# Kernel tuning notes

Hardware: AMD Instinct MI355X
Metric: run time of the kernel (lower is better)

Reference implementation:

```python
import jax, jax.numpy as jnp
import numpy as np

INF = 1.0e10
EPS = 1e-12

def setup_inputs() -> dict:
    key = jax.random.key(0)
    k1, k2 = jax.random.split(key)
    B, N, A = 512, 16384, 64
    return {
        "residue_ca_pos": jax.random.normal(k1, (B, N, 3), dtype=jnp.float32) * 10.0,
        "residue_mask": jnp.ones((B, N), dtype=jnp.float32),
        "atom_pos": jax.random.normal(k2, (B, A, 3), dtype=jnp.float32) * 10.0,
        "atom_mask": jnp.ones((B, A), dtype=jnp.float32),
        "max_p": 1,
        "top_k": 4096,
    }

def reference(residue_ca_pos, residue_mask, atom_pos, atom_mask, max_p, top_k):
    # ligand centroid per batch: [B, 3]
    centroid = atom_pos.sum(-2) / atom_mask.sum(-1, keepdims=True)
    # distance from centroid to each residue Ca, invalid residues pushed to +inf
    diff = centroid[:, None, :] - residue_ca_pos            # [B, N, 3]
    dists = jnp.sqrt(jnp.sum(diff * diff, axis=-1) + EPS) + (1.0 - residue_mask) * INF
    # k smallest distances -> neighbor indices [B, top_k]
    _, nbr_indices = jax.lax.top_k(-dists, top_k)
    rows = jnp.arange(residue_mask.shape[0])[:, None]       # [B, 1]
    # scatter writes building the masks (faithful to torch scatter_ with constants)
    residue_spatial_mask = residue_mask.at[rows, nbr_indices].set(0.0)
    residue_spatial_mask_esm = (1.0 - residue_mask).at[rows, nbr_indices].set(32.0)
    return residue_spatial_mask, residue_spatial_mask_esm
```

## Files before the change

### kernel.cpp

```cpp
#include <hip/hip_runtime.h>

#pragma clang fp contract(off)

#define B_   512
#define N_   16384
#define A_   64
#define TPB  1024
#define NW   16
#define CAP  2048

#define AS1 __attribute__((address_space(1)))
#define AS3 __attribute__((address_space(3)))

__device__ __forceinline__ void gl2lds16(const float* g, float* l) {
    __builtin_amdgcn_global_load_lds((const AS1 unsigned int*)g,
                                     (AS3 unsigned int*)l, 16, 0, 0);
}

__global__ __launch_bounds__(TPB) void fused_kernel(
    const float* __restrict__ pos,   const float* __restrict__ mask,
    const float* __restrict__ apos,  const float* __restrict__ amask,
    const int*   __restrict__ topk_ptr,
    float* __restrict__ out0, float* __restrict__ out1)
{
#pragma clang fp contract(off)
    __shared__ __align__(16) float wbuf[NW][2][1024];
    __shared__ unsigned       hist[2048];
    __shared__ unsigned       hist2[32];
    __shared__ unsigned       cand_bits[CAP];
    __shared__ unsigned short cand_idx[CAP];
    __shared__ unsigned char  sel_flags[CAP];
    __shared__ float          s_atoms[A_ * 3 + A_];
    __shared__ unsigned s_B11, s_less11, s_P16, s_j, s_ncand, s_k;

    const int tid = threadIdx.x;
    const int w   = tid >> 6;
    const int l   = tid & 63;
    const int b   = blockIdx.x;
    const float* __restrict__ p = pos  + (size_t)b * N_ * 3;
    const float* __restrict__ m = mask + (size_t)b * N_;

    hist[tid]        = 0u;
    hist[tid + 1024] = 0u;
    if (tid < 32) hist2[tid] = 0u;
    if (tid < 256)
        s_atoms[tid] = (tid < 192) ? apos[(size_t)b * 192 + tid]
                                   : amask[(size_t)b * 64 + (tid - 192)];
    if (tid == 0) {
        s_ncand = 0u;
        int kk = *topk_ptr;
        if (kk < 0)  kk = 0;
        if (kk > N_) kk = N_;
        s_k = (unsigned)kk;
    }
    __syncthreads();

#define ISSUE_SUB(S, BUFIDX) do {                                          \
        const float* ps_ = p + (size_t)(w * 1024 + (S) * 256) * 3;         \
        float* dst_ = &wbuf[w][(BUFIDX)][0];                               \
        gl2lds16(ps_ + 4 * l,        dst_ + 4 * l);                        \
        gl2lds16(ps_ + 256 + 4 * l,  dst_ + 256 + 4 * l);                  \
        gl2lds16(ps_ + 512 + 4 * l,  dst_ + 512 + 4 * l);                  \
        gl2lds16(m + w * 1024 + (S) * 256 + 4 * l, dst_ + 768 + 4 * l);    \
    } while (0)

    ISSUE_SUB(0, 0);
    ISSUE_SUB(1, 1);

    float cx, cy, cz;
    {
        float comp = 0.0f, ms = 0.0f;
        if (l < 3) {
            comp = s_atoms[l];
            for (int a = 1; a < A_; ++a) comp += s_atoms[a * 3 + l];
        }
        if (l == 3) {
            const float* am = s_atoms + 192;
            float r0 = am[0], r1 = am[1], r2 = am[2], r3 = am[3];
            float r4 = am[4], r5 = am[5], r6 = am[6], r7 = am[7];
            for (int i = 8; i < A_; i += 8) {
                r0 += am[i + 0]; r1 += am[i + 1]; r2 += am[i + 2]; r3 += am[i + 3];
                r4 += am[i + 4]; r5 += am[i + 5]; r6 += am[i + 6]; r7 += am[i + 7];
            }
            ms = ((r0 + r1) + (r2 + r3)) + ((r4 + r5) + (r6 + r7));
        }
        ms = __shfl(ms, 3, 64);
        const float cc = (l < 3) ? comp / ms : 0.0f;
        cx = __shfl(cc, 0, 64);
        cy = __shfl(cc, 1, 64);
        cz = __shfl(cc, 2, 64);
    }

    const unsigned k = s_k;

    unsigned rbits[16];
    float    rmv[16];

#define DO_ELEM(S, J, PX, PY, PZ, MM) do {                                 \
        float dx_ = cx - (PX), dy_ = cy - (PY), dz_ = cz - (PZ);           \
        float s_ = (dx_ * dx_ + dy_ * dy_) + dz_ * dz_;                    \
        s_ = s_ + 1e-12f;                                                  \
        float d_ = sqrtf(s_);                                              \
        d_ = d_ + (1.0f - (MM)) * 1e10f;                                   \
        const unsigned bits_ = __float_as_uint(d_);                        \
        rbits[(S) * 4 + (J)] = bits_;                                      \
        rmv[(S) * 4 + (J)]   = (MM);                                       \
        atomicAdd(&hist[bits_ >> 21], 1u);                                 \
    } while (0)

#pragma unroll
    for (int s = 0; s < 4; ++s) {
        if (s < 3) asm volatile("s_waitcnt vmcnt(4)" ::: "memory");
        else       asm volatile("s_waitcnt vmcnt(0)" ::: "memory");
        __builtin_amdgcn_sched_barrier(0);

        const float* buf = &wbuf[w][s & 1][0];
        const float4 q0 = *(const float4*)(buf + 12 * l);
        const float4 q1 = *(const float4*)(buf + 12 * l + 4);
        const float4 q2 = *(const float4*)(buf + 12 * l + 8);
        const float4 mv = *(const float4*)(buf + 768 + 4 * l);

        DO_ELEM(s, 0, q0.x, q0.y, q0.z, mv.x);
        DO_ELEM(s, 1, q0.w, q1.x, q1.y, mv.y);
        DO_ELEM(s, 2, q1.z, q1.w, q2.x, mv.z);
        DO_ELEM(s, 3, q2.y, q2.z, q2.w, mv.w);

        asm volatile("s_waitcnt lgkmcnt(0)" ::: "memory");
        __builtin_amdgcn_sched_barrier(0);
        if (s + 2 < 4) ISSUE_SUB(s + 2, s & 1);
    }
    __syncthreads();

    if (k > 0) {
        if (tid < 64) {
            unsigned s = 0;
#pragma unroll
            for (int i = 0; i < 32; ++i) s += hist[tid * 32 + i];
            unsigned incl = s;
#pragma unroll
            for (int off = 1; off < 64; off <<= 1) {
                unsigned v = (unsigned)__shfl_up((int)incl, off, 64);
                if (tid >= off) incl += v;
            }
            unsigned long long bal = __ballot(incl >= k);
            const int g = __ffsll(bal) - 1;
            const unsigned cum1 = (unsigned)__shfl((int)(incl - s), g, 64);

            unsigned h2 = (tid < 32) ? hist[g * 32 + tid] : 0u;
            unsigned incl2 = h2;
#pragma unroll
            for (int off = 1; off < 64; off <<= 1) {
                unsigned v = (unsigned)__shfl_up((int)incl2, off, 64);
                if (tid >= off) incl2 += v;
            }
            unsigned long long bal2 = __ballot(tid < 32 && (cum1 + incl2 >= k));
            const int sb = __ffsll(bal2) - 1;
            const unsigned cum2 = cum1 + (unsigned)__shfl((int)(incl2 - h2), sb, 64);
            if (tid == 0) { s_B11 = (unsigned)(g * 32 + sb); s_less11 = cum2; }
        }
        __syncthreads();
        const unsigned B11 = s_B11;

#pragma unroll
        for (int x = 0; x < 16; ++x) {
            const unsigned v = rbits[x] >> 16;
            if ((v >> 5) == B11) atomicAdd(&hist2[v & 31u], 1u);
        }
        __syncthreads();
        if (tid < 64) {
            unsigned h = (tid < 32) ? hist2[tid] : 0u;
            unsigned incl = h;
#pragma unroll
            for (int off = 1; off < 64; off <<= 1) {
                unsigned v = (unsigned)__shfl_up((int)incl, off, 64);
                if (tid >= off) incl += v;
            }
            const unsigned less11 = s_less11;
            unsigned long long bal = __ballot(tid < 32 && (less11 + incl >= k));
            const int sb = __ffsll(bal) - 1;
            const unsigned cumx = less11 + (unsigned)__shfl((int)(incl - h), sb, 64);
            if (tid == 0) { s_P16 = (B11 << 5) | (unsigned)sb; s_j = k - cumx; }
        }
        __syncthreads();
        const unsigned P16 = s_P16;
        const unsigned j   = s_j;

#pragma unroll
        for (int x = 0; x < 16; ++x) {
            const unsigned bits = rbits[x];
            if ((bits >> 16) == P16) {
                const unsigned wr = atomicAdd(&s_ncand, 1u);
                if (wr < CAP) {
                    cand_bits[wr] = bits;
                    cand_idx[wr]  = (unsigned short)(w * 1024 + (x >> 2) * 256
                                                     + 4 * l + (x & 3));
                    rbits[x] = 0xFFFF0000u | wr;
                }
            }
        }
        __syncthreads();

        const unsigned cnum = min(s_ncand, (unsigned)CAP);
        for (unsigned t = tid; t < cnum; t += TPB) {
            const unsigned bt = cand_bits[t];
            const unsigned it = cand_idx[t];
            unsigned rank = 0;
            for (unsigned u = 0; u < cnum; ++u) {
                const unsigned bu = cand_bits[u];
                rank += (bu < bt) || (bu == bt && (unsigned)cand_idx[u] < it);
            }
            sel_flags[t] = (rank < j) ? (unsigned char)1 : (unsigned char)0;
        }
        __syncthreads();
    }

    const unsigned P16f = (k > 0) ? s_P16 : 0u;
#pragma unroll
    for (int s = 0; s < 4; ++s) {
        float4 o0, o1;
        float* o0p = &o0.x; float* o1p = &o1.x;
#pragma unroll
        for (int jj = 0; jj < 4; ++jj) {
            const unsigned v   = rbits[s * 4 + jj];
            const unsigned v16 = v >> 16;
            bool sel = false;
            if (k > 0) {
                sel = (v16 == 0xFFFFu) ? (sel_flags[v & (CAP - 1u)] != 0)
                                       : (v16 < P16f);
            }
            const float mvv = rmv[s * 4 + jj];
            o0p[jj] = sel ? 0.0f  : mvv;
            o1p[jj] = sel ? 32.0f : (1.0f - mvv);
        }
        const size_t o = (size_t)b * N_ + w * 1024 + s * 256 + 4 * l;
        *(float4*)(out0 + o) = o0;
        *(float4*)(out1 + o) = o1;
    }
}

extern "C" void kernel_launch(void* const* d_in, const int* in_sizes, int n_in,
                              void* d_out, int out_size, void* d_ws, size_t ws_size,
                              hipStream_t stream) {
    const float* pos   = (const float*)d_in[0];
    const float* rmask = (const float*)d_in[1];
    const float* apos  = (const float*)d_in[2];
    const float* amask = (const float*)d_in[3];
    const int*   topk  = (const int*)d_in[5];

    float* out0 = (float*)d_out;
    float* out1 = out0 + (size_t)B_ * N_;

    fused_kernel<<<B_, TPB, 0, stream>>>(pos, rmask, apos, amask, topk, out0, out1);
}
```

Measured before the change: 212.9 us.

## Process two batch rows per block, prefetching second row into LDS during selection

Each block now handles two batch rows. The first row is loaded directly into registers. Meanwhile, half of the second row plus its atoms is prefetched into a 128 KB LDS stage buffer, so those loads overlap the first row's radix selection. The goal is to hide the memory latency behind the serial select phase. The cost is half as many blocks (256 on 256 CUs), a larger LDS footprint, and a longer serial chain per block.

```diff
diff --git a/kernel.cpp b/kernel.cpp
--- a/kernel.cpp
+++ b/kernel.cpp
@@ -6,8 +6,8 @@
 #define N_   16384
 #define A_   64
 #define TPB  1024
-#define NW   16
 #define CAP  2048
+#define STAGE_F 32768
 
 #define AS1 __attribute__((address_space(1)))
 #define AS3 __attribute__((address_space(3)))
@@ -15,6 +15,152 @@
 __device__ __forceinline__ void gl2lds16(const float* g, float* l) {
     __builtin_amdgcn_global_load_lds((const AS1 unsigned int*)g,
                                      (AS3 unsigned int*)l, 16, 0, 0);
+}
+
+#define RAWBAR() do { asm volatile("s_waitcnt lgkmcnt(0)" ::: "memory"); \
+                      __builtin_amdgcn_s_barrier();                      \
+                      asm volatile("" ::: "memory"); } while (0)
+
+__device__ __forceinline__ void centroid_wave(const float* sa, const int l,
+                                              float& cx, float& cy, float& cz) {
+    float comp = 0.0f, ms = 0.0f;
+    if (l < 3) {
+        comp = sa[l];
+        for (int a = 1; a < A_; ++a) comp += sa[a * 3 + l];
+    }
+    if (l == 3) {
+        const float* am = sa + 192;
+        float r0 = am[0], r1 = am[1], r2 = am[2], r3 = am[3];
+        float r4 = am[4], r5 = am[5], r6 = am[6], r7 = am[7];
+        for (int i = 8; i < A_; i += 8) {
+            r0 += am[i + 0]; r1 += am[i + 1]; r2 += am[i + 2]; r3 += am[i + 3];
+            r4 += am[i + 4]; r5 += am[i + 5]; r6 += am[i + 6]; r7 += am[i + 7];
+        }
+        ms = ((r0 + r1) + (r2 + r3)) + ((r4 + r5) + (r6 + r7));
+    }
+    ms = __shfl(ms, 3, 64);
+    const float cc = (l < 3) ? comp / ms : 0.0f;
+    cx = __shfl(cc, 0, 64);
+    cy = __shfl(cc, 1, 64);
+    cz = __shfl(cc, 2, 64);
+}
+
+__device__ __forceinline__ unsigned run_select(
+    unsigned (&rbits)[16], const unsigned k, const int tid,
+    unsigned* hist, unsigned* hist2, unsigned* cand_bits,
+    unsigned short* cand_idx, unsigned char* sel_flags,
+    unsigned* s_B11, unsigned* s_less11, unsigned* s_P16, unsigned* s_j,
+    unsigned* s_ncand)
+{
+    if (k == 0) return 0u;
+    if (tid < 64) {
+        unsigned s = 0;
+#pragma unroll
+        for (int i = 0; i < 32; ++i) s += hist[tid * 32 + i];
+        unsigned incl = s;
+#pragma unroll
+        for (int off = 1; off < 64; off <<= 1) {
+            unsigned v = (unsigned)__shfl_up((int)incl, off, 64);
+            if (tid >= off) incl += v;
+        }
+        unsigned long long bal = __ballot(incl >= k);
+        const int g = __ffsll(bal) - 1;
+        const unsigned cum1 = (unsigned)__shfl((int)(incl - s), g, 64);
+
+        unsigned h2 = (tid < 32) ? hist[g * 32 + tid] : 0u;
+        unsigned incl2 = h2;
+#pragma unroll
+        for (int off = 1; off < 64; off <<= 1) {
+            unsigned v = (unsigned)__shfl_up((int)incl2, off, 64);
+            if (tid >= off) incl2 += v;
+        }
+        unsigned long long bal2 = __ballot(tid < 32 && (cum1 + incl2 >= k));
+        const int sb = __ffsll(bal2) - 1;
+        const unsigned cum2 = cum1 + (unsigned)__shfl((int)(incl2 - h2), sb, 64);
+        if (tid == 0) { *s_B11 = (unsigned)(g * 32 + sb); *s_less11 = cum2; }
+    }
+    RAWBAR();
+    const unsigned B11 = *s_B11;
+
+#pragma unroll
+    for (int x = 0; x < 16; ++x) {
+        const unsigned v = rbits[x] >> 16;
+        if ((v >> 5) == B11) atomicAdd(&hist2[v & 31u], 1u);
+    }
+    RAWBAR();
+    if (tid < 64) {
+        unsigned h = (tid < 32) ? hist2[tid] : 0u;
+        unsigned incl = h;
+#pragma unroll
+        for (int off = 1; off < 64; off <<= 1) {
+            unsigned v = (unsigned)__shfl_up((int)incl, off, 64);
+            if (tid >= off) incl += v;
+        }
+        const unsigned less11 = *s_less11;
+        unsigned long long bal = __ballot(tid < 32 && (less11 + incl >= k));
+        const int sb = __ffsll(bal) - 1;
+        const unsigned cumx = less11 + (unsigned)__shfl((int)(incl - h), sb, 64);
+        if (tid == 0) { *s_P16 = (B11 << 5) | (unsigned)sb; *s_j = k - cumx; }
+    }
+    RAWBAR();
+    const unsigned P16 = *s_P16;
+    const unsigned j   = *s_j;
+
+#pragma unroll
+    for (int x = 0; x < 16; ++x) {
+        const unsigned bits = rbits[x];
+        if ((bits >> 16) == P16) {
+            const unsigned wr = atomicAdd(s_ncand, 1u);
+            if (wr < CAP) {
+                cand_bits[wr] = bits;
+                cand_idx[wr]  = (unsigned short)((x >> 2) * 4096 + tid * 4 + (x & 3));
+                rbits[x] = 0xFFFF0000u | wr;
+            }
+        }
+    }
+    RAWBAR();
+
+    const unsigned cnum = min(*s_ncand, (unsigned)CAP);
+    for (unsigned t = tid; t < cnum; t += TPB) {
+        const unsigned bt = cand_bits[t];
+        const unsigned it = cand_idx[t];
+        unsigned rank = 0;
+        for (unsigned u = 0; u < cnum; ++u) {
+            const unsigned bu = cand_bits[u];
+            rank += (bu < bt) || (bu == bt && (unsigned)cand_idx[u] < it);
+        }
+        sel_flags[t] = (rank < j) ? (unsigned char)1 : (unsigned char)0;
+    }
+    RAWBAR();
+    return P16;
+}
+
+__device__ __forceinline__ void write_masks(
+    const unsigned (&rbits)[16], const float (&rmv)[16],
+    const unsigned P16f, const unsigned k, const unsigned char* sel_flags,
+    float* out0, float* out1, const size_t base, const int tid)
+{
+#pragma unroll
+    for (int it = 0; it < 4; ++it) {
+        const int i0 = it * 4096 + tid * 4;
+        float4 o0, o1;
+        float* o0p = &o0.x; float* o1p = &o1.x;
+#pragma unroll
+        for (int jj = 0; jj < 4; ++jj) {
+            const unsigned v   = rbits[it * 4 + jj];
+            const unsigned v16 = v >> 16;
+            bool sel = false;
+            if (k > 0) {
+                sel = (v16 == 0xFFFFu) ? (sel_flags[v & (CAP - 1u)] != 0)
+                                       : (v16 < P16f);
+            }
+            const float mvv = rmv[it * 4 + jj];
+            o0p[jj] = sel ? 0.0f  : mvv;
+            o1p[jj] = sel ? 32.0f : (1.0f - mvv);
+        }
+        *(float4*)(out0 + base + i0) = o0;
+        *(float4*)(out1 + base + i0) = o1;
+    }
 }
 
 __global__ __launch_bounds__(TPB) void fused_kernel(
@@ -24,28 +170,31 @@
     float* __restrict__ out0, float* __restrict__ out1)
 {
 #pragma clang fp contract(off)
-    __shared__ __align__(16) float wbuf[NW][2][1024];
+    __shared__ __align__(16) float stage[STAGE_F];
     __shared__ unsigned       hist[2048];
     __shared__ unsigned       hist2[32];
     __shared__ unsigned       cand_bits[CAP];
     __shared__ unsigned short cand_idx[CAP];
     __shared__ unsigned char  sel_flags[CAP];
-    __shared__ float          s_atoms[A_ * 3 + A_];
+    __shared__ float          s_atoms[256];
+    __shared__ __align__(16) float s_atoms2[256];
     __shared__ unsigned s_B11, s_less11, s_P16, s_j, s_ncand, s_k;
 
     const int tid = threadIdx.x;
-    const int w   = tid >> 6;
     const int l   = tid & 63;
-    const int b   = blockIdx.x;
-    const float* __restrict__ p = pos  + (size_t)b * N_ * 3;
-    const float* __restrict__ m = mask + (size_t)b * N_;
+    const int b0  = 2 * blockIdx.x;
+    const int b1  = b0 + 1;
+    const float* __restrict__ p0 = pos  + (size_t)b0 * N_ * 3;
+    const float* __restrict__ m0 = mask + (size_t)b0 * N_;
+    const float* __restrict__ p1 = pos  + (size_t)b1 * N_ * 3;
+    const float* __restrict__ m1 = mask + (size_t)b1 * N_;
 
     hist[tid]        = 0u;
     hist[tid + 1024] = 0u;
     if (tid < 32) hist2[tid] = 0u;
     if (tid < 256)
-        s_atoms[tid] = (tid < 192) ? apos[(size_t)b * 192 + tid]
-                                   : amask[(size_t)b * 64 + (tid - 192)];
+        s_atoms[tid] = (tid < 192) ? apos[(size_t)b0 * 192 + tid]
+                                   : amask[(size_t)b0 * 64 + (tid - 192)];
     if (tid == 0) {
         s_ncand = 0u;
         int kk = *topk_ptr;
@@ -55,187 +204,104 @@
     }
     __syncthreads();
 
-#define ISSUE_SUB(S, BUFIDX) do {                                          \
-        const float* ps_ = p + (size_t)(w * 1024 + (S) * 256) * 3;         \
-        float* dst_ = &wbuf[w][(BUFIDX)][0];                               \
-        gl2lds16(ps_ + 4 * l,        dst_ + 4 * l);                        \
-        gl2lds16(ps_ + 256 + 4 * l,  dst_ + 256 + 4 * l);                  \
-        gl2lds16(ps_ + 512 + 4 * l,  dst_ + 512 + 4 * l);                  \
-        gl2lds16(m + w * 1024 + (S) * 256 + 4 * l, dst_ + 768 + 4 * l);    \
-    } while (0)
-
-    ISSUE_SUB(0, 0);
-    ISSUE_SUB(1, 1);
-
     float cx, cy, cz;
-    {
-        float comp = 0.0f, ms = 0.0f;
-        if (l < 3) {
-            comp = s_atoms[l];
-            for (int a = 1; a < A_; ++a) comp += s_atoms[a * 3 + l];
-        }
-        if (l == 3) {
-            const float* am = s_atoms + 192;
-            float r0 = am[0], r1 = am[1], r2 = am[2], r3 = am[3];
-            float r4 = am[4], r5 = am[5], r6 = am[6], r7 = am[7];
-            for (int i = 8; i < A_; i += 8) {
-                r0 += am[i + 0]; r1 += am[i + 1]; r2 += am[i + 2]; r3 += am[i + 3];
-                r4 += am[i + 4]; r5 += am[i + 5]; r6 += am[i + 6]; r7 += am[i + 7];
-            }
-            ms = ((r0 + r1) + (r2 + r3)) + ((r4 + r5) + (r6 + r7));
-        }
-        ms = __shfl(ms, 3, 64);
-        const float cc = (l < 3) ? comp / ms : 0.0f;
-        cx = __shfl(cc, 0, 64);
-        cy = __shfl(cc, 1, 64);
-        cz = __shfl(cc, 2, 64);
-    }
-
+    centroid_wave(s_atoms, l, cx, cy, cz);
     const unsigned k = s_k;
 
     unsigned rbits[16];
     float    rmv[16];
 
-#define DO_ELEM(S, J, PX, PY, PZ, MM) do {                                 \
+#define DO_ELEM(IT, J, PX, PY, PZ, MM) do {                                \
         float dx_ = cx - (PX), dy_ = cy - (PY), dz_ = cz - (PZ);           \
-        float s_ = (dx_ * dx_ + dy_ * dy_) + dz_ * dz_;                    \
-        s_ = s_ + 1e-12f;                                                  \
-        float d_ = sqrtf(s_);                                              \
+        float s2_ = (dx_ * dx_ + dy_ * dy_) + dz_ * dz_;                   \
+        s2_ = s2_ + 1e-12f;                                                \
+        float d_ = sqrtf(s2_);                                             \
         d_ = d_ + (1.0f - (MM)) * 1e10f;                                   \
         const unsigned bits_ = __float_as_uint(d_);                        \
-        rbits[(S) * 4 + (J)] = bits_;                                      \
-        rmv[(S) * 4 + (J)]   = (MM);                                       \
+        rbits[(IT) * 4 + (J)] = bits_;                                     \
+        rmv[(IT) * 4 + (J)]   = (MM);                                      \
         atomicAdd(&hist[bits_ >> 21], 1u);                                 \
     } while (0)
 
-#pragma unroll
-    for (int s = 0; s < 4; ++s) {
-        if (s < 3) asm volatile("s_waitcnt vmcnt(4)" ::: "memory");
-        else       asm volatile("s_waitcnt vmcnt(0)" ::: "memory");
-        __builtin_amdgcn_sched_barrier(0);
-
-        const float* buf = &wbuf[w][s & 1][0];
-        const float4 q0 = *(const float4*)(buf + 12 * l);
-        const float4 q1 = *(const float4*)(buf + 12 * l + 4);
-        const float4 q2 = *(const float4*)(buf + 12 * l + 8);
-        const float4 mv = *(const float4*)(buf + 768 + 4 * l);
-
-        DO_ELEM(s, 0, q0.x, q0.y, q0.z, mv.x);
-        DO_ELEM(s, 1, q0.w, q1.x, q1.y, mv.y);
-        DO_ELEM(s, 2, q1.z, q1.w, q2.x, mv.z);
-        DO_ELEM(s, 3, q2.y, q2.z, q2.w, mv.w);
-
-        asm volatile("s_waitcnt lgkmcnt(0)" ::: "memory");
-        __builtin_amdgcn_sched_barrier(0);
-        if (s + 2 < 4) ISSUE_SUB(s + 2, s & 1);
-    }
-    __syncthreads();
-
-    if (k > 0) {
-        if (tid < 64) {
-            unsigned s = 0;
-#pragma unroll
-            for (int i = 0; i < 32; ++i) s += hist[tid * 32 + i];
-            unsigned incl = s;
-#pragma unroll
-            for (int off = 1; off < 64; off <<= 1) {
-                unsigned v = (unsigned)__shfl_up((int)incl, off, 64);
-                if (tid >= off) incl += v;
-            }
-            unsigned long long bal = __ballot(incl >= k);
-            const int g = __ffsll(bal) - 1;
-            const unsigned cum1 = (unsigned)__shfl((int)(incl - s), g, 64);
-
-            unsigned h2 = (tid < 32) ? hist[g * 32 + tid] : 0u;
-            unsigned incl2 = h2;
-#pragma unroll
-            for (int off = 1; off < 64; off <<= 1) {
-                unsigned v = (unsigned)__shfl_up((int)incl2, off, 64);
-                if (tid >= off) incl2 += v;
-            }
-            unsigned long long bal2 = __ballot(tid < 32 && (cum1 + incl2 >= k));
-            const int sb = __ffsll(bal2) - 1;
-            const unsigned cum2 = cum1 + (unsigned)__shfl((int)(incl2 - h2), sb, 64);
-            if (tid == 0) { s_B11 = (unsigned)(g * 32 + sb); s_less11 = cum2; }
-        }
-        __syncthreads();
-        const unsigned B11 = s_B11;
-
-#pragma unroll
-        for (int x = 0; x < 16; ++x) {
-            const unsigned v = rbits[x] >> 16;
-            if ((v >> 5) == B11) atomicAdd(&hist2[v & 31u], 1u);
-        }
-        __syncthreads();
-        if (tid < 64) {
-            unsigned h = (tid < 32) ? hist2[tid] : 0u;
-            unsigned incl = h;
-#pragma unroll
-            for (int off = 1; off < 64; off <<= 1) {
-                unsigned v = (unsigned)__shfl_up((int)incl, off, 64);
-                if (tid >= off) incl += v;
-            }
-            const unsigned less11 = s_less11;
-            unsigned long long bal = __ballot(tid < 32 && (less11 + incl >= k));
-            const int sb = __ffsll(bal) - 1;
-            const unsigned cumx = less11 + (unsigned)__shfl((int)(incl - h), sb, 64);
-            if (tid == 0) { s_P16 = (B11 << 5) | (unsigned)sb; s_j = k - cumx; }
-        }
-        __syncthreads();
-        const unsigned P16 = s_P16;
-        const unsigned j   = s_j;
-
-#pragma unroll
-        for (int x = 0; x < 16; ++x) {
-            const unsigned bits = rbits[x];
-            if ((bits >> 16) == P16) {
-                const unsigned wr = atomicAdd(&s_ncand, 1u);
-                if (wr < CAP) {
-                    cand_bits[wr] = bits;
-                    cand_idx[wr]  = (unsigned short)(w * 1024 + (x >> 2) * 256
-                                                     + 4 * l + (x & 3));
-                    rbits[x] = 0xFFFF0000u | wr;
-                }
-            }
-        }
-        __syncthreads();
-
-        const unsigned cnum = min(s_ncand, (unsigned)CAP);
-        for (unsigned t = tid; t < cnum; t += TPB) {
-            const unsigned bt = cand_bits[t];
-            const unsigned it = cand_idx[t];
-            unsigned rank = 0;
-            for (unsigned u = 0; u < cnum; ++u) {
-                const unsigned bu = cand_bits[u];
-                rank += (bu < bt) || (bu == bt && (unsigned)cand_idx[u] < it);
-            }
-            sel_flags[t] = (rank < j) ? (unsigned char)1 : (unsigned char)0;
-        }
-        __syncthreads();
-    }
-
-    const unsigned P16f = (k > 0) ? s_P16 : 0u;
-#pragma unroll
-    for (int s = 0; s < 4; ++s) {
-        float4 o0, o1;
-        float* o0p = &o0.x; float* o1p = &o1.x;
-#pragma unroll
-        for (int jj = 0; jj < 4; ++jj) {
-            const unsigned v   = rbits[s * 4 + jj];
-            const unsigned v16 = v >> 16;
-            bool sel = false;
-            if (k > 0) {
-                sel = (v16 == 0xFFFFu) ? (sel_flags[v & (CAP - 1u)] != 0)
-                                       : (v16 < P16f);
-            }
-            const float mvv = rmv[s * 4 + jj];
-            o0p[jj] = sel ? 0.0f  : mvv;
-            o1p[jj] = sel ? 32.0f : (1.0f - mvv);
-        }
-        const size_t o = (size_t)b * N_ + w * 1024 + s * 256 + 4 * l;
-        *(float4*)(out0 + o) = o0;
-        *(float4*)(out1 + o) = o1;
-    }
+#define DO4(IT, PA, PB, PC, MV) do {                                       \
+        DO_ELEM(IT, 0, (PA).x, (PA).y, (PA).z, (MV).x);                    \
+        DO_ELEM(IT, 1, (PA).w, (PB).x, (PB).y, (MV).y);                    \
+        DO_ELEM(IT, 2, (PB).z, (PB).w, (PC).x, (MV).z);                    \
+        DO_ELEM(IT, 3, (PC).y, (PC).z, (PC).w, (MV).w);                    \
+    } while (0)
+
+#pragma unroll
+    for (int it = 0; it < 4; ++it) {
+        const int i0 = it * 4096 + tid * 4;
+        const float4 pa = *(const float4*)(p0 + (size_t)i0 * 3);
+        const float4 pb = *(const float4*)(p0 + (size_t)i0 * 3 + 4);
+        const float4 pc = *(const float4*)(p0 + (size_t)i0 * 3 + 8);
+        const float4 mv = *(const float4*)(m0 + i0);
+        DO4(it, pa, pb, pc, mv);
+    }
+
+#pragma unroll
+    for (int q = 0; q < 8; ++q) {
+        const int f = q * 4096 + tid * 4;
+        const float* src = (q < 6) ? (p1 + f) : (m1 + (f - 24576));
+        gl2lds16(src, &stage[f]);
+    }
+    if (tid < 64) {
+        const float* src = (l < 48) ? (apos + (size_t)b1 * 192 + 4 * l)
+                                    : (amask + (size_t)b1 * 64 + (4 * l - 192));
+        gl2lds16(src, &s_atoms2[4 * l]);
+    }
+    RAWBAR();
+
+    const unsigned P16_0 = run_select(rbits, k, tid, hist, hist2, cand_bits,
+                                      cand_idx, sel_flags, &s_B11, &s_less11,
+                                      &s_P16, &s_j, &s_ncand);
+
+    asm volatile("s_waitcnt vmcnt(0)" ::: "memory");
+    __builtin_amdgcn_s_barrier();
+    __builtin_amdgcn_sched_barrier(0);
+
+    write_masks(rbits, rmv, P16_0, k, sel_flags, out0, out1,
+                (size_t)b0 * N_, tid);
+
+    hist[tid]        = 0u;
+    hist[tid + 1024] = 0u;
+    if (tid < 32) hist2[tid] = 0u;
+    if (tid == 0) s_ncand = 0u;
+    centroid_wave(s_atoms2, l, cx, cy, cz);
+    RAWBAR();
+
+    {
+        const int i2 = 2 * 4096 + tid * 4;
+        const int i3 = 3 * 4096 + tid * 4;
+        const float4 pa2 = *(const float4*)(p1 + (size_t)i2 * 3);
+        const float4 pb2 = *(const float4*)(p1 + (size_t)i2 * 3 + 4);
+        const float4 pc2 = *(const float4*)(p1 + (size_t)i2 * 3 + 8);
+        const float4 mv2 = *(const float4*)(m1 + i2);
+        const float4 pa3 = *(const float4*)(p1 + (size_t)i3 * 3);
+        const float4 pb3 = *(const float4*)(p1 + (size_t)i3 * 3 + 4);
+        const float4 pc3 = *(const float4*)(p1 + (size_t)i3 * 3 + 8);
+        const float4 mv3 = *(const float4*)(m1 + i3);
+
+#pragma unroll
+        for (int it = 0; it < 2; ++it) {
+            const int g = it * 4096 + tid * 4;
+            const float4 pa = *(const float4*)&stage[g * 3];
+            const float4 pb = *(const float4*)&stage[g * 3 + 4];
+            const float4 pc = *(const float4*)&stage[g * 3 + 8];
+            const float4 mv = *(const float4*)&stage[24576 + g];
+            DO4(it, pa, pb, pc, mv);
+        }
+        DO4(2, pa2, pb2, pc2, mv2);
+        DO4(3, pa3, pb3, pc3, mv3);
+    }
+    RAWBAR();
+
+    const unsigned P16_1 = run_select(rbits, k, tid, hist, hist2, cand_bits,
+                                      cand_idx, sel_flags, &s_B11, &s_less11,
+                                      &s_P16, &s_j, &s_ncand);
+    write_masks(rbits, rmv, P16_1, k, sel_flags, out0, out1,
+                (size_t)b1 * N_, tid);
 }
 
 extern "C" void kernel_launch(void* const* d_in, const int* in_sizes, int n_in,
@@ -250,5 +316,6 @@
     float* out0 = (float*)d_out;
     float* out1 = out0 + (size_t)B_ * N_;
 
-    fused_kernel<<<B_, TPB, 0, stream>>>(pos, rmask, apos, amask, topk, out0, out1);
-}
+    fused_kernel<<<B_ / 2, TPB, 0, stream>>>(pos, rmask, apos, amask, topk,
+                                             out0, out1);
+}
```

Result: no change. 212.1 us (-0.4%).
